# Performance work log

Hardware: AMD Instinct MI355X
Metric: run time of the kernel (lower is better)

## Reference

```python
import jax, jax.numpy as jnp
import numpy as np
import math

B, S = 2, 2048
D_IN = 512
D_OUT = 512
P = 8
K = 8


def setup_inputs() -> dict:
    key = jax.random.key(0)
    ks = jax.random.split(key, 8)
    mean_phi = math.log(math.sqrt(2.0 / (D_IN * K)))
    mean_w2 = math.log(math.sqrt(2.0 / D_OUT))
    x = jax.random.normal(ks[0], (B, S, D_IN), dtype=jnp.float32)
    phi_raw = mean_phi + 0.2 * jax.random.normal(ks[1], (D_OUT, D_IN * K), dtype=jnp.float32)
    phi_bias = jnp.zeros((D_OUT,), dtype=jnp.float32)
    raw_weight2 = mean_w2 + 0.2 * jax.random.normal(ks[2], (P, D_OUT, D_OUT), dtype=jnp.float32)
    bias2 = jnp.zeros((P, D_OUT), dtype=jnp.float32)
    gate_raw2 = jnp.full((P,), -3.0, dtype=jnp.float32)
    # kaiming_uniform with a=sqrt(5) on shape (P, 2*D_in, D_out): fan_in = 2*D_in
    bound = math.sqrt(6.0 / ((1.0 + 5.0) * (2 * D_IN)))
    z_weight = jax.random.uniform(ks[3], (P, 2 * D_IN, D_OUT), dtype=jnp.float32,
                                  minval=-bound, maxval=bound)
    gate_raw = jnp.full((P,), -3.0, dtype=jnp.float32)
    output_bias = jnp.zeros((P, D_OUT), dtype=jnp.float32)
    return {
        "x": x, "phi_raw": phi_raw, "phi_bias": phi_bias,
        "raw_weight2": raw_weight2, "bias2": bias2, "gate_raw2": gate_raw2,
        "z_weight": z_weight, "gate_raw": gate_raw, "output_bias": output_bias,
    }


def reference(x, phi_raw, phi_bias, raw_weight2, bias2, gate_raw2,
              z_weight, gate_raw, output_bias):
    sp = jax.nn.softplus
    orig = x.shape
    x_flat = x.reshape(-1, D_IN)                              # [N, Din]
    N = x_flat.shape[0]
    shifts = jnp.linspace(-1.0, 1.0, K, dtype=x.dtype)        # [k]
    phi = sp(x_flat[:, :, None] + shifts[None, None, :])      # [N, Din, k]
    phi_flat = phi.reshape(N, D_IN * K)                       # [N, Din*k]
    # PositiveLinearHK: weight = softplus(raw)^2
    w_phi = jnp.square(sp(phi_raw))                           # [Dout, Din*k]
    x_proj = phi_flat @ w_phi.T + phi_bias                    # [N, Dout]
    g1 = jax.nn.sigmoid(gate_raw)[:, None, None]              # [P,1,1]
    z0 = sp(x_proj[None, :, :] * g1)                          # [P, N, Dout]
    w2 = jnp.square(sp(raw_weight2))                          # [P, Dout, Dout]
    # bmm(z0, w2.transpose(1,2)) == einsum over the second Dout axis of w2
    z1 = jnp.einsum('pnd,ped->pne', z0, w2) + bias2[:, None, :]
    g2 = jax.nn.sigmoid(gate_raw2)[:, None, None]
    z1 = sp(z1 * g2)                                          # [P, N, Dout]
    x_res_in = jnp.concatenate([x_flat, x_flat], axis=-1)     # [N, 2*Din]
    x_res = jnp.einsum('nc,pce->pne', x_res_in, z_weight)     # [P, N, Dout]
    z_final = sp(z1 + x_res) + output_bias[:, None, :]        # [P, N, Dout]
    out = jnp.transpose(z_final, (1, 0, 2))                   # [N, P, Dout]
    return out.reshape(tuple(orig[:-1]) + (P, D_OUT))
```

## Files before the change

### kernel.cpp

```cpp
#include <hip/hip_runtime.h>

typedef unsigned short u16;
typedef __attribute__((ext_vector_type(8))) short bf16x8;
typedef __attribute__((ext_vector_type(4))) float floatx4;
typedef __attribute__((ext_vector_type(8))) unsigned short u16x8;
typedef __attribute__((ext_vector_type(4))) unsigned short u16x4;

#define NTOK 4096
#define DDIN 512
#define DDOUT 512
#define NP 8
#define SPLITK 8

__device__ __forceinline__ float b2f(u16 b) {
    union { unsigned int u; float f; } v; v.u = ((unsigned int)b) << 16; return v.f;
}
__device__ __forceinline__ u16 f2b(float f) {
    union { float f; unsigned int u; } v; v.f = f;
    unsigned int r = (v.u + 0x7fffu + ((v.u >> 16) & 1u)) >> 16;
    return (u16)r;
}
__device__ __forceinline__ float sp(float x) {
    return fmaxf(x, 0.f) + __logf(1.f + __expf(-fabsf(x)));
}
__device__ __forceinline__ float sigm(float x) { return 1.f / (1.f + __expf(-x)); }

__device__ __forceinline__ void gld16(const u16* g, u16* l) {
    __builtin_amdgcn_global_load_lds((const __attribute__((address_space(1))) void*)g,
                                     (__attribute__((address_space(3))) void*)l, 16, 0, 0);
}


__global__ void prep_sqsp2(const float* __restrict__ in1, u16* __restrict__ out1, int n1,
                           const float* __restrict__ in2, u16* __restrict__ out2, int n2) {
    int i = blockIdx.x * 256 + threadIdx.x;
    if (i < n1) {
        float s = sp(in1[i]);
        out1[i] = f2b(s * s);
    } else if (i - n1 < n2) {
        int j = i - n1;
        float s = sp(in2[j]);
        out2[j] = f2b(s * s);
    }
}

__global__ void prep_zwT(const float* __restrict__ zw, u16* __restrict__ zwT) {
    int p = blockIdx.z;
    int c0 = blockIdx.x * 32, e0 = blockIdx.y * 32;
    __shared__ float tb[32][33];
    int tx = threadIdx.x, ty = threadIdx.y;
    const float* base = zw + (size_t)p * 1024 * 512;
#pragma unroll
    for (int r = 0; r < 4; ++r) {
        int cl = ty * 4 + r;
        float a = base[(size_t)(c0 + cl) * 512 + e0 + tx];
        float b = base[(size_t)(c0 + cl + 512) * 512 + e0 + tx];
        tb[cl][tx] = a + b;
    }
    __syncthreads();
    u16* outb = zwT + (size_t)p * 512 * 512;
#pragma unroll
    for (int r = 0; r < 4; ++r) {
        int el = ty * 4 + r;
        outb[(size_t)(e0 + el) * 512 + c0 + tx] = f2b(tb[tx][el]);
    }
}

__global__ void phi_kernel(const float* __restrict__ x, u16* __restrict__ phi,
                           u16* __restrict__ xb) {
    int i = blockIdx.x * 256 + threadIdx.x;
    float xv = x[i];
    xb[i] = f2b(xv);
    u16x8 v;
#pragma unroll
    for (int k = 0; k < 8; ++k) {
        float s = -1.f + (2.f / 7.f) * (float)k;
        v[k] = f2b(sp(xv + s));
    }
    *(u16x8*)(phi + (size_t)i * 8) = v;
}

__launch_bounds__(256, 3)
__global__ void gemm1p(const u16* __restrict__ phi, const u16* __restrict__ wphi,
                       u16* __restrict__ xpart) {
    __shared__ __align__(16) u16 lds[2 * 8192];
    u16* As = lds;
    u16* Bs = lds + 8192;

    const int id = blockIdx.x;
    const int kc = id & 7;
    const int local = id >> 3;
    const int o0 = (local & 3) * 128;
    const int n0 = (local >> 2) * 128;
    const int kbase = kc * 512;

    const int t = threadIdx.x;
    const int wave = t >> 6, lane = t & 63;
    const int wm = wave >> 1, wn = wave & 1;
    const int l15 = lane & 15, quad = lane >> 4;
    const int srow = t >> 3;
    const int sgx = (((t & 7) ^ (srow & 7))) * 8;

    floatx4 acc[4][4];
#pragma unroll
    for (int i = 0; i < 4; ++i)
#pragma unroll
        for (int j = 0; j < 4; ++j) acc[i][j] = {0.f, 0.f, 0.f, 0.f};

    for (int k0 = 0; k0 < 512; k0 += 64) {
        const u16* ga = phi + (size_t)(n0 + srow) * 4096 + kbase + k0 + sgx;
        const u16* gb = wphi + (size_t)(o0 + srow) * 4096 + kbase + k0 + sgx;
        __syncthreads();
#pragma unroll
        for (int c = 0; c < 4; ++c) {
            gld16(ga + (size_t)c * 32 * 4096, As + c * 2048 + t * 8);
            gld16(gb + (size_t)c * 32 * 4096, Bs + c * 2048 + t * 8);
        }
        __syncthreads();
#pragma unroll
        for (int ks = 0; ks < 2; ++ks) {
            bf16x8 a[4], b[4];
#pragma unroll
            for (int s = 0; s < 4; ++s) {
                int ra = wm * 64 + s * 16 + l15;
                int rb = wn * 64 + s * 16 + l15;
                a[s] = *(const bf16x8*)(As + ra * 64 + (((ks * 4 + quad) ^ (ra & 7)) * 8));
                b[s] = *(const bf16x8*)(Bs + rb * 64 + (((ks * 4 + quad) ^ (rb & 7)) * 8));
            }
#pragma unroll
            for (int sm = 0; sm < 4; ++sm)
#pragma unroll
                for (int sn = 0; sn < 4; ++sn)
                    acc[sm][sn] = __builtin_amdgcn_mfma_f32_16x16x32_bf16(a[sm], b[sn], acc[sm][sn], 0, 0, 0);
        }
    }

    u16* xp = xpart + (size_t)kc * NTOK * DDOUT;
#pragma unroll
    for (int sm = 0; sm < 4; ++sm)
#pragma unroll
        for (int sn = 0; sn < 4; ++sn) {
            int gcol = o0 + wn * 64 + sn * 16 + l15;
#pragma unroll
            for (int r = 0; r < 4; ++r) {
                int grow = n0 + wm * 64 + sm * 16 + quad * 4 + r;
                xp[(size_t)grow * DDOUT + gcol] = f2b(acc[sm][sn][r]);
            }
        }
}

__global__ void reduce_ep(const u16* __restrict__ xpart, const float* __restrict__ phi_bias,
                          const float* __restrict__ gate_raw, u16* __restrict__ z0) {
    int idx = blockIdx.x * 256 + threadIdx.x;
    int n = idx >> 6;
    int o8 = (idx & 63) * 8;
    size_t base = (size_t)n * DDOUT + o8;
    float s[8];
#pragma unroll
    for (int j = 0; j < 8; ++j) s[j] = 0.f;
#pragma unroll
    for (int kc = 0; kc < SPLITK; ++kc) {
        u16x8 v = *(const u16x8*)(xpart + (size_t)kc * NTOK * DDOUT + base);
#pragma unroll
        for (int j = 0; j < 8; ++j) s[j] += b2f(v[j]);
    }
#pragma unroll
    for (int j = 0; j < 8; ++j) s[j] += phi_bias[o8 + j];
#pragma unroll
    for (int p = 0; p < NP; ++p) {
        float g = sigm(gate_raw[p]);
        u16x8 v;
#pragma unroll
        for (int j = 0; j < 8; ++j) v[j] = f2b(sp(s[j] * g));
        *(u16x8*)(z0 + (size_t)p * NTOK * DDOUT + base) = v;
    }
}

__launch_bounds__(512, 2)
__global__ void gemm23(const u16* __restrict__ z0, const u16* __restrict__ w2b,
                       const u16* __restrict__ xb, const u16* __restrict__ zwT,
                       const float* __restrict__ bias2, const float* __restrict__ gate_raw2,
                       const float* __restrict__ output_bias, float* __restrict__ out) {
    __shared__ __align__(16) u16 lds[2 * 4 * 8192];

    const int id = blockIdx.x;
    const int p = id & 7;
    const int local = id >> 3;
    const int e0 = (local & 3) * 128;
    const int n0 = (local >> 2) * 128;

    const int t = threadIdx.x;
    const int wave = t >> 6, lane = t & 63;
    const int wm = wave & 1, wn = wave >> 1;
    const int l15 = lane & 15, quad = lane >> 4;
    const int srow = t >> 3;
    const int sgx = ((t & 7) ^ (srow & 7)) * 8;

    const u16* gA1 = z0  + (size_t)p * NTOK * DDOUT + (size_t)(n0 + srow) * 512 + sgx;
    const u16* gB1 = w2b + (size_t)p * DDOUT * DDOUT + (size_t)(e0 + srow) * 512 + sgx;
    const u16* gA2 = xb  + (size_t)(n0 + srow) * 512 + sgx;
    const u16* gB2 = zwT + (size_t)p * DDOUT * DDIN + (size_t)(e0 + srow) * 512 + sgx;

    floatx4 acc1[4][2], acc2[4][2];
#pragma unroll
    for (int i = 0; i < 4; ++i)
#pragma unroll
        for (int j = 0; j < 2; ++j) {
            acc1[i][j] = {0.f, 0.f, 0.f, 0.f};
            acc2[i][j] = {0.f, 0.f, 0.f, 0.f};
        }

    auto STAGE = [&](int b, int k0) {
        u16* L = lds + b * 32768;
#pragma unroll
        for (int c = 0; c < 2; ++c) {
            gld16(gA1 + k0 + c * 64 * 512, L + c * 4096 + t * 8);
            gld16(gB1 + k0 + c * 64 * 512, L + 8192 + c * 4096 + t * 8);
            gld16(gA2 + k0 + c * 64 * 512, L + 16384 + c * 4096 + t * 8);
            gld16(gB2 + k0 + c * 64 * 512, L + 24576 + c * 4096 + t * 8);
        }
    };

    STAGE(0, 0);
    for (int it = 0; it < 8; ++it) {
        const int cur = it & 1;
        __syncthreads();
        if (it < 7) STAGE(cur ^ 1, (it + 1) * 64);
        const u16* A1 = lds + cur * 32768;
        const u16* B1 = A1 + 8192;
        const u16* A2 = A1 + 16384;
        const u16* B2 = A1 + 24576;
#pragma unroll
        for (int ks = 0; ks < 2; ++ks) {
            bf16x8 a1[4], b1[2], a2[4], b2[2];
#pragma unroll
            for (int s = 0; s < 4; ++s) {
                int ra = wm * 64 + s * 16 + l15;
                int ko = ((ks * 4 + quad) ^ (ra & 7)) * 8;
                a1[s] = *(const bf16x8*)(A1 + ra * 64 + ko);
                a2[s] = *(const bf16x8*)(A2 + ra * 64 + ko);
            }
#pragma unroll
            for (int s = 0; s < 2; ++s) {
                int rb = wn * 32 + s * 16 + l15;
                int ko = ((ks * 4 + quad) ^ (rb & 7)) * 8;
                b1[s] = *(const bf16x8*)(B1 + rb * 64 + ko);
                b2[s] = *(const bf16x8*)(B2 + rb * 64 + ko);
            }
#pragma unroll
            for (int sm = 0; sm < 4; ++sm)
#pragma unroll
                for (int sn = 0; sn < 2; ++sn) {
                    acc1[sm][sn] = __builtin_amdgcn_mfma_f32_16x16x32_bf16(a1[sm], b1[sn], acc1[sm][sn], 0, 0, 0);
                    acc2[sm][sn] = __builtin_amdgcn_mfma_f32_16x16x32_bf16(a2[sm], b2[sn], acc2[sm][sn], 0, 0, 0);
                }
        }
    }

    const float g2p = sigm(gate_raw2[p]);
#pragma unroll
    for (int sm = 0; sm < 4; ++sm)
#pragma unroll
        for (int sn = 0; sn < 2; ++sn) {
            int gcol = e0 + wn * 32 + sn * 16 + l15;
            float bb = bias2[p * DDOUT + gcol];
            float ob = output_bias[p * DDOUT + gcol];
#pragma unroll
            for (int r = 0; r < 4; ++r) {
                int grow = n0 + wm * 64 + sm * 16 + quad * 4 + r;
                float v1 = acc1[sm][sn][r] + bb;
                float o = sp(sp(v1 * g2p) + acc2[sm][sn][r]) + ob;
                out[(size_t)grow * (NP * DDOUT) + p * DDOUT + gcol] = o;
            }
        }
}

extern "C" void kernel_launch(void* const* d_in, const int* in_sizes, int n_in,
                              void* d_out, int out_size, void* d_ws, size_t ws_size,
                              hipStream_t stream) {
    const float* x           = (const float*)d_in[0];
    const float* phi_raw     = (const float*)d_in[1];
    const float* phi_bias    = (const float*)d_in[2];
    const float* raw_weight2 = (const float*)d_in[3];
    const float* bias2       = (const float*)d_in[4];
    const float* gate_raw2   = (const float*)d_in[5];
    const float* z_weight    = (const float*)d_in[6];
    const float* gate_raw    = (const float*)d_in[7];
    const float* output_bias = (const float*)d_in[8];
    float* out = (float*)d_out;

    u16* ws   = (u16*)d_ws;
    u16* phi  = ws;
    u16* wphi = phi + (size_t)4096 * 4096;
    u16* w2b  = wphi + (size_t)512 * 4096;
    u16* zwT  = w2b + (size_t)8 * 512 * 512;
    u16* z0   = zwT + (size_t)8 * 512 * 512;
    u16* xb   = z0 + (size_t)8 * 4096 * 512;
    u16* xpart = (u16*)d_out;

    const int n1 = 512 * 4096, n2 = 8 * 512 * 512;
    hipLaunchKernelGGL(prep_sqsp2, dim3((n1 + n2) / 256), dim3(256), 0, stream,
                       phi_raw, wphi, n1, raw_weight2, w2b, n2);
    hipLaunchKernelGGL(prep_zwT, dim3(16, 16, 8), dim3(32, 8), 0, stream, z_weight, zwT);
    hipLaunchKernelGGL(phi_kernel, dim3(8192), dim3(256), 0, stream, x, phi, xb);
    hipLaunchKernelGGL(gemm1p, dim3(1024), dim3(256), 0, stream, phi, wphi, xpart);
    hipLaunchKernelGGL(reduce_ep, dim3(1024), dim3(256), 0, stream, xpart, phi_bias, gate_raw, z0);
    hipLaunchKernelGGL(gemm23, dim3(1024), dim3(512), 0, stream,
                       z0, w2b, xb, zwT, bias2, gate_raw2, output_bias, out);
}
```

Before: 215.4 us.

## Fuse per-path gate softplus into gemm23 A-operand staging instead of materializing z0

The reduce kernel now writes a single bf16 x_proj (4096x512) instead of eight gated softplus copies z0 (8x4096x512). gemm23 loads x_proj tiles into registers, applies sigmoid-gate scaling and softplus, and writes the result to LDS after the MFMA loop, which removes the large z0 write and read. In exchange each gemm23 block recomputes the softplus for its tile (repeated across the four e0 column tiles) and uses a register-staged path that occupies extra VGPRs and issue slots. It also adds a second bf16 rounding of x_proj before the gate, which slightly changes numerics.

```diff
diff --git a/kernel.cpp b/kernel.cpp
--- a/kernel.cpp
+++ b/kernel.cpp
@@ -149,8 +149,8 @@
         }
 }
 
-__global__ void reduce_ep(const u16* __restrict__ xpart, const float* __restrict__ phi_bias,
-                          const float* __restrict__ gate_raw, u16* __restrict__ z0) {
+__global__ void reduce_xp(const u16* __restrict__ xpart, const float* __restrict__ phi_bias,
+                          u16* __restrict__ xproj) {
     int idx = blockIdx.x * 256 + threadIdx.x;
     int n = idx >> 6;
     int o8 = (idx & 63) * 8;
@@ -164,23 +164,18 @@
 #pragma unroll
         for (int j = 0; j < 8; ++j) s[j] += b2f(v[j]);
     }
-#pragma unroll
-    for (int j = 0; j < 8; ++j) s[j] += phi_bias[o8 + j];
-#pragma unroll
-    for (int p = 0; p < NP; ++p) {
-        float g = sigm(gate_raw[p]);
-        u16x8 v;
-#pragma unroll
-        for (int j = 0; j < 8; ++j) v[j] = f2b(sp(s[j] * g));
-        *(u16x8*)(z0 + (size_t)p * NTOK * DDOUT + base) = v;
-    }
+    u16x8 v;
+#pragma unroll
+    for (int j = 0; j < 8; ++j) v[j] = f2b(s[j] + phi_bias[o8 + j]);
+    *(u16x8*)(xproj + base) = v;
 }
 
 __launch_bounds__(512, 2)
-__global__ void gemm23(const u16* __restrict__ z0, const u16* __restrict__ w2b,
+__global__ void gemm23(const u16* __restrict__ xproj, const u16* __restrict__ w2b,
                        const u16* __restrict__ xb, const u16* __restrict__ zwT,
                        const float* __restrict__ bias2, const float* __restrict__ gate_raw2,
-                       const float* __restrict__ output_bias, float* __restrict__ out) {
+                       const float* __restrict__ gate_raw, const float* __restrict__ output_bias,
+                       float* __restrict__ out) {
     __shared__ __align__(16) u16 lds[2 * 4 * 8192];
 
     const int id = blockIdx.x;
@@ -196,7 +191,9 @@
     const int srow = t >> 3;
     const int sgx = ((t & 7) ^ (srow & 7)) * 8;
 
-    const u16* gA1 = z0  + (size_t)p * NTOK * DDOUT + (size_t)(n0 + srow) * 512 + sgx;
+    const float g1p = sigm(gate_raw[p]);
+
+    const u16* gXP = xproj + (size_t)(n0 + srow) * 512 + sgx;
     const u16* gB1 = w2b + (size_t)p * DDOUT * DDOUT + (size_t)(e0 + srow) * 512 + sgx;
     const u16* gA2 = xb  + (size_t)(n0 + srow) * 512 + sgx;
     const u16* gB2 = zwT + (size_t)p * DDOUT * DDIN + (size_t)(e0 + srow) * 512 + sgx;
@@ -210,22 +207,43 @@
             acc2[i][j] = {0.f, 0.f, 0.f, 0.f};
         }
 
-    auto STAGE = [&](int b, int k0) {
+    auto STAGE_GLD = [&](int b, int k0) {
         u16* L = lds + b * 32768;
 #pragma unroll
         for (int c = 0; c < 2; ++c) {
-            gld16(gA1 + k0 + c * 64 * 512, L + c * 4096 + t * 8);
             gld16(gB1 + k0 + c * 64 * 512, L + 8192 + c * 4096 + t * 8);
             gld16(gA2 + k0 + c * 64 * 512, L + 16384 + c * 4096 + t * 8);
             gld16(gB2 + k0 + c * 64 * 512, L + 24576 + c * 4096 + t * 8);
         }
     };
 
-    STAGE(0, 0);
+    u16x8 xa0, xa1;
+    auto A1_LOAD = [&](int k0) {
+        xa0 = *(const u16x8*)(gXP + k0);
+        xa1 = *(const u16x8*)(gXP + k0 + 64 * 512);
+    };
+    auto A1_WRITE = [&](int b) {
+        u16* L = lds + b * 32768;
+        u16x8 v0, v1;
+#pragma unroll
+        for (int j = 0; j < 8; ++j) {
+            v0[j] = f2b(sp(b2f(xa0[j]) * g1p));
+            v1[j] = f2b(sp(b2f(xa1[j]) * g1p));
+        }
+        *(u16x8*)(L + t * 8) = v0;
+        *(u16x8*)(L + 4096 + t * 8) = v1;
+    };
+
+    A1_LOAD(0);
+    STAGE_GLD(0, 0);
+    A1_WRITE(0);
     for (int it = 0; it < 8; ++it) {
         const int cur = it & 1;
         __syncthreads();
-        if (it < 7) STAGE(cur ^ 1, (it + 1) * 64);
+        if (it < 7) {
+            A1_LOAD((it + 1) * 64);
+            STAGE_GLD(cur ^ 1, (it + 1) * 64);
+        }
         const u16* A1 = lds + cur * 32768;
         const u16* B1 = A1 + 8192;
         const u16* A2 = A1 + 16384;
@@ -255,6 +273,7 @@
                     acc2[sm][sn] = __builtin_amdgcn_mfma_f32_16x16x32_bf16(a2[sm], b2[sn], acc2[sm][sn], 0, 0, 0);
                 }
         }
+        if (it < 7) A1_WRITE(cur ^ 1);
     }
 
     const float g2p = sigm(gate_raw2[p]);
@@ -294,8 +313,8 @@
     u16* wphi = phi + (size_t)4096 * 4096;
     u16* w2b  = wphi + (size_t)512 * 4096;
     u16* zwT  = w2b + (size_t)8 * 512 * 512;
-    u16* z0   = zwT + (size_t)8 * 512 * 512;
-    u16* xb   = z0 + (size_t)8 * 4096 * 512;
+    u16* xproj = zwT + (size_t)8 * 512 * 512;
+    u16* xb   = xproj + (size_t)4096 * 512;
     u16* xpart = (u16*)d_out;
 
     const int n1 = 512 * 4096, n2 = 8 * 512 * 512;
@@ -304,7 +323,7 @@
     hipLaunchKernelGGL(prep_zwT, dim3(16, 16, 8), dim3(32, 8), 0, stream, z_weight, zwT);
     hipLaunchKernelGGL(phi_kernel, dim3(8192), dim3(256), 0, stream, x, phi, xb);
     hipLaunchKernelGGL(gemm1p, dim3(1024), dim3(256), 0, stream, phi, wphi, xpart);
-    hipLaunchKernelGGL(reduce_ep, dim3(1024), dim3(256), 0, stream, xpart, phi_bias, gate_raw, z0);
+    hipLaunchKernelGGL(reduce_xp, dim3(1024), dim3(256), 0, stream, xpart, phi_bias, xproj);
     hipLaunchKernelGGL(gemm23, dim3(1024), dim3(512), 0, stream,
-                       z0, w2b, xb, zwT, bias2, gate_raw2, output_bias, out);
-}
+                       xproj, w2b, xb, zwT, bias2, gate_raw2, gate_raw, output_bias, out);
+}
```

Measured after the change: 250.3 us. 16.2% more time.
